# Kernel tuning notes

Measured on AMD Instinct MI355X. Metric: run time of the kernel, lower is better.

Reference implementation:

```python
import jax, jax.numpy as jnp
import numpy as np

QLEN, MLEN, BSZ, DM, NH, DH, DI = 512, 512, 8, 1024, 16, 64, 4096
KLEN = QLEN + MLEN
EPS = 1e-5
NEG = -1e30


def layer_norm(x, g, b):
    mu = jnp.mean(x, axis=-1, keepdims=True)
    var = jnp.mean(jnp.square(x - mu), axis=-1, keepdims=True)
    return (x - mu) * jax.lax.rsqrt(var + EPS) * g + b


def rel_shift(x):
    # x: [qlen, rlen, bsz, n_head] -> Transformer-XL relative shift
    q, r, b, n = x.shape
    zp = jnp.zeros((q, 1, b, n), x.dtype)
    xp = jnp.concatenate([zp, x], axis=1).reshape(r + 1, q, b, n)
    return xp[1:].reshape(q, r, b, n)


def setup_inputs() -> dict:
    key = jax.random.key(0)
    ks = jax.random.split(key, 12)
    inp = {
        "w": jax.random.normal(ks[0], (QLEN, BSZ, DM), jnp.float32),
        "r": jax.random.normal(ks[1], (KLEN, DM), jnp.float32),
        "mems": jax.random.normal(ks[2], (MLEN, BSZ, DM), jnp.float32),
        "w_qkv": jax.random.normal(ks[3], (DM, 3 * NH * DH), jnp.float32) * 0.02,
        "w_r": jax.random.normal(ks[4], (DM, NH * DH), jnp.float32) * 0.02,
        "w_o": jax.random.normal(ks[5], (NH * DH, DM), jnp.float32) * 0.02,
        "r_w_bias": jax.random.normal(ks[6], (NH, DH), jnp.float32) * 0.02,
        "r_r_bias": jax.random.normal(ks[7], (NH, DH), jnp.float32) * 0.02,
        "ln1_g": jnp.ones((DM,), jnp.float32),
        "ln1_b": jnp.zeros((DM,), jnp.float32),
        "ff_w1": jax.random.normal(ks[8], (DM, DI), jnp.float32) * 0.02,
        "ff_b1": jnp.zeros((DI,), jnp.float32),
        "ff_w2": jax.random.normal(ks[9], (DI, DM), jnp.float32) * 0.02,
        "ff_b2": jnp.zeros((DM,), jnp.float32),
        "ln2_g": jnp.ones((DM,), jnp.float32),
        "ln2_b": jnp.zeros((DM,), jnp.float32),
    }
    # causal mask with memory: query i (global pos MLEN+i) cannot attend to j > MLEN+i
    i = jnp.arange(QLEN)[:, None]
    j = jnp.arange(KLEN)[None, :]
    inp["attn_mask"] = j > (i + MLEN)
    return inp


def reference(w, r, mems, attn_mask, w_qkv, w_r, w_o, r_w_bias, r_r_bias,
              ln1_g, ln1_b, ff_w1, ff_b1, ff_w2, ff_b2, ln2_g, ln2_b):
    qlen, bsz = w.shape[0], w.shape[1]
    scale = 1.0 / (DH ** 0.5)
    cat = jnp.concatenate([mems, w], axis=0)                 # [klen, b, d]
    klen = cat.shape[0]
    heads = cat @ w_qkv                                      # [klen, b, 3*H*D]
    hq, hk, hv = jnp.split(heads, 3, axis=-1)
    hq = hq[-qlen:].reshape(qlen, bsz, NH, DH)
    hk = hk.reshape(klen, bsz, NH, DH)
    hv = hv.reshape(klen, bsz, NH, DH)
    r_head_k = (r @ w_r).reshape(klen, NH, DH)               # [rlen, H, D]

    AC = jnp.einsum('ibnd,jbnd->ijbn', hq + r_w_bias, hk)
    BD = rel_shift(jnp.einsum('ibnd,jnd->ijbn', hq + r_r_bias, r_head_k))
    score = (AC + BD) * scale                                # [q, k, b, h]
    score = jnp.where(attn_mask[:, :, None, None], NEG, score)
    prob = jax.nn.softmax(score, axis=1)
    vec = jnp.einsum('ijbn,jbnd->ibnd', prob, hv).reshape(qlen, bsz, NH * DH)
    attn_out = vec @ w_o
    h = layer_norm(w + attn_out, ln1_g, ln1_b)               # post-LN
    ff = jax.nn.relu(h @ ff_w1 + ff_b1) @ ff_w2 + ff_b2
    return layer_norm(h + ff, ln2_g, ln2_b)
```

## Files before the change

kernel.cpp:

```cpp
#include <hip/hip_runtime.h>
#include <hip/hip_bf16.h>

#define QLEN 512
#define MLEN 512
#define KLEN 1024
#define BSZ 8
#define DM 1024
#define NH 16
#define DH 64
#define DI 4096
#define NEGF (-1e30f)
#define HM_PART ((size_t)8388608)

typedef unsigned short u16;
typedef __attribute__((ext_vector_type(8))) short short8;
typedef __attribute__((ext_vector_type(4))) short s16x4;
typedef __attribute__((ext_vector_type(4))) float f32x4;

__device__ __forceinline__ float bf2f(u16 u) {
    union { unsigned i; float f; } x; x.i = ((unsigned)u) << 16; return x.f;
}
__device__ __forceinline__ u16 f2bf(float f) {
    __hip_bfloat16 h = __float2bfloat16(f);
    return *reinterpret_cast<u16*>(&h);
}
__device__ __forceinline__ float4 ldg4(const float* p) {
    return *reinterpret_cast<const float4*>(p);
}
__device__ __forceinline__ void gload16(const void* g, void* l) {
    __builtin_amdgcn_global_load_lds(
        (const __attribute__((address_space(1))) void*)g,
        (__attribute__((address_space(3))) void*)l, 16, 0, 0);
}

__global__ __launch_bounds__(256) void cast2_kernel(
    const float* __restrict__ a, const float* __restrict__ b, int splitE,
    u16* __restrict__ out, int n)
{
    int idx = (blockIdx.x * 256 + threadIdx.x) * 4;
    if (idx >= n) return;
    const float* src = (idx < splitE) ? (a + idx) : (b + (idx - splitE));
    float4 v = ldg4(src);
    u16 o[4] = { f2bf(v.x), f2bf(v.y), f2bf(v.z), f2bf(v.w) };
    *reinterpret_cast<uint2*>(&out[idx]) = *reinterpret_cast<uint2*>(o);
}

__device__ __forceinline__ void tr32(
    const float* __restrict__ W, u16* __restrict__ WT, int K, int N, int k0, int n0)
{
    __shared__ float tile[32][33];
    const int tx = threadIdx.x & 31, ty = threadIdx.x >> 5;
    #pragma unroll
    for (int j = 0; j < 4; ++j)
        tile[ty + j * 8][tx] = W[(size_t)(k0 + ty + j * 8) * N + n0 + tx];
    __syncthreads();
    #pragma unroll
    for (int j = 0; j < 4; ++j)
        WT[(size_t)(n0 + ty + j * 8) * K + k0 + tx] = f2bf(tile[tx][ty + j * 8]);
}

__global__ __launch_bounds__(256) void transpose_all(
    const float* __restrict__ w_qkv, u16* __restrict__ qkvT,
    const float* __restrict__ w_r,   u16* __restrict__ wrT,
    const float* __restrict__ w_o,   u16* __restrict__ woT,
    const float* __restrict__ ffw1,  u16* __restrict__ f1T,
    const float* __restrict__ ffw2,  u16* __restrict__ f2T)
{
    int id = blockIdx.x;
    if (id < 3072)       { int l = id;        tr32(w_qkv, qkvT, 1024, 3072, (l / 96) * 32, (l % 96) * 32); }
    else if (id < 4096)  { int l = id - 3072; tr32(w_r,   wrT,  1024, 1024, (l / 32) * 32, (l % 32) * 32); }
    else if (id < 5120)  { int l = id - 4096; tr32(w_o,   woT,  1024, 1024, (l / 32) * 32, (l % 32) * 32); }
    else if (id < 9216)  { int l = id - 5120; tr32(ffw1,  f1T,  1024, 4096, (l / 128) * 32, (l % 128) * 32); }
    else                 { int l = id - 9216; tr32(ffw2,  f2T,  4096, 1024, (l / 32) * 32, (l % 32) * 32); }
}

__global__ __launch_bounds__(256) void v_transpose(
    const u16* __restrict__ Vhm, u16* __restrict__ Vg)
{
    const int bn = blockIdx.x;
    const int kt = blockIdx.y;
    const int t = threadIdx.x;
    __shared__ u16 L[64 * 64];

    #pragma unroll
    for (int rep = 0; rep < 2; ++rep) {
        int idx = t + rep * 256;
        int key = idx >> 3, dc = (idx & 7) * 8;
        short8 v = *reinterpret_cast<const short8*>(
            &Vhm[((size_t)bn * 1024 + kt * 64 + key) * 64 + dc]);
        *reinterpret_cast<short8*>((char*)L + key * 128 + ((dc * 2) ^ ((key & 7) << 4))) = v;
    }
    __syncthreads();
    #pragma unroll
    for (int rep = 0; rep < 2; ++rep) {
        int idx = t + rep * 256;
        int d = idx >> 3, kc = (idx & 7) * 8;
        short8 o;
        #pragma unroll
        for (int e = 0; e < 8; ++e)
            o[e] = *(const short*)((char*)L + (kc + e) * 128 + ((d * 2) ^ (((kc + e) & 7) << 4)));
        *reinterpret_cast<short8*>(&Vg[((size_t)(bn * 64 + d)) * KLEN + kt * 64 + kc]) = o;
    }
}

template<bool BIAS, bool RELU, int OUT>
__global__ __launch_bounds__(256) void gemm_mfma(
    const u16* __restrict__ A, const u16* __restrict__ BT,
    const float* __restrict__ bias,
    float* __restrict__ Cf, u16* __restrict__ Cb,
    int M, int N, int K, int lda, int ldb)
{
    __shared__ u16 As[128 * 64];
    __shared__ u16 Bs[128 * 64];
    const int bm = blockIdx.y * 128, bn = blockIdx.x * 128;
    const int z = blockIdx.z;
    A  += (size_t)z * K;
    BT += (size_t)z * K;
    const size_t zoff = (size_t)z * M * N;
    const int t = threadIdx.x;
    const int w = t >> 6, l = t & 63, lg = l >> 4, lq = l & 15;
    const int wm = (w >> 1) * 64, wn = (w & 1) * 64;
    const int r8 = l >> 3, slot = l & 7;
    const int gcol = (slot * 16) ^ (r8 << 4);

    f32x4 acc[4][4];
    #pragma unroll
    for (int x = 0; x < 4; ++x)
        #pragma unroll
        for (int y = 0; y < 4; ++y)
            acc[x][y] = (f32x4){0.f, 0.f, 0.f, 0.f};

    const int swzr = (lq & 7) << 4;

    for (int k0 = 0; k0 < K; k0 += 64) {
        __syncthreads();
        #pragma unroll
        for (int it = 0; it < 4; ++it) {
            const int base_row = w * 8 + it * 32;
            gload16((const char*)A + (((size_t)(bm + base_row + r8) * lda + k0) << 1) + gcol,
                    (char*)As + base_row * 128);
            gload16((const char*)BT + (((size_t)(bn + base_row + r8) * ldb + k0) << 1) + gcol,
                    (char*)Bs + base_row * 128);
        }
        __syncthreads();
        #pragma unroll
        for (int ks = 0; ks < 2; ++ks) {
            const int cb = (ks * 64 + 16 * lg) ^ swzr;
            short8 af[4], bf_[4];
            #pragma unroll
            for (int x = 0; x < 4; ++x)
                af[x] = *reinterpret_cast<const short8*>((char*)As + (wm + 16 * x + lq) * 128 + cb);
            #pragma unroll
            for (int y = 0; y < 4; ++y)
                bf_[y] = *reinterpret_cast<const short8*>((char*)Bs + (wn + 16 * y + lq) * 128 + cb);
            #pragma unroll
            for (int x = 0; x < 4; ++x)
                #pragma unroll
                for (int y = 0; y < 4; ++y)
                    acc[x][y] = __builtin_amdgcn_mfma_f32_16x16x32_bf16(af[x], bf_[y], acc[x][y], 0, 0, 0);
        }
    }
    const int nn = ((bn + wn) >> 6) & 15;
    #pragma unroll
    for (int x = 0; x < 4; ++x) {
        #pragma unroll
        for (int y = 0; y < 4; ++y) {
            const int col = bn + wn + 16 * y + lq;
            #pragma unroll
            for (int r = 0; r < 4; ++r) {
                const int row = bm + wm + 16 * x + 4 * lg + r;
                float v = acc[x][y][r];
                if constexpr (BIAS) { if (z == 0) v += bias[col]; }
                if constexpr (RELU) v = fmaxf(v, 0.f);
                if constexpr (OUT == 0) Cf[zoff + (size_t)row * N + col] = v;
                else if constexpr (OUT == 1) Cb[zoff + (size_t)row * N + col] = f2bf(v);
                else
                    Cb[((size_t)nn * 1024 + row) * 64 + 16 * y + lq] = f2bf(v);
            }
        }
    }
}

template<bool BIAS, bool RELU, int OUT>
__global__ __launch_bounds__(512, 2) void gemm_deep(
    const u16* __restrict__ A, const u16* __restrict__ BT,
    const float* __restrict__ bias,
    float* __restrict__ Cf, u16* __restrict__ Cb,
    int M, int N, int K, int lda, int ldb)
{
    __shared__ u16 lds[3 * 24576];
    const int bm = blockIdx.y * 256, bn = blockIdx.x * 128;
    const int z = blockIdx.z;
    A  += (size_t)z * K;
    BT += (size_t)z * K;
    const size_t zoff = (size_t)z * M * N;
    const int t = threadIdx.x;
    const int w = t >> 6, l = t & 63, lg = l >> 4, lq = l & 15;
    const int wm = (w >> 1) * 64;
    const int wn = (w & 1) * 64;
    const int srow = t >> 3, slot = t & 7;
    const int gcol = (slot * 16) ^ ((srow & 7) << 4);
    const int swzr = (lq & 7) << 4;

    auto stage_tile = [&](int kt, int buf) {
        const int k0 = kt * 64;
        char* Ab = (char*)lds + buf * 49152 + w * 1024;
        char* Bb = (char*)lds + buf * 49152 + 32768 + w * 1024;
        #pragma unroll
        for (int i = 0; i < 4; ++i)
            gload16((const char*)A + (((size_t)(bm + i * 64 + srow) * lda + k0) << 1) + gcol,
                    Ab + i * 8192);
        #pragma unroll
        for (int i = 0; i < 2; ++i)
            gload16((const char*)BT + (((size_t)(bn + i * 64 + srow) * ldb + k0) << 1) + gcol,
                    Bb + i * 8192);
    };

    f32x4 acc[4][4];
    #pragma unroll
    for (int x = 0; x < 4; ++x)
        #pragma unroll
        for (int y = 0; y < 4; ++y)
            acc[x][y] = (f32x4){0.f, 0.f, 0.f, 0.f};

    const int NT = K >> 6;
    stage_tile(0, 0);
    stage_tile(1, 1);

    for (int kt = 0; kt < NT; ++kt) {
        if (kt < NT - 1) asm volatile("s_waitcnt vmcnt(6)" ::: "memory");
        else             asm volatile("s_waitcnt vmcnt(0)" ::: "memory");
        __builtin_amdgcn_s_barrier();
        __builtin_amdgcn_sched_barrier(0);
        if (kt + 2 < NT) stage_tile(kt + 2, (kt + 2) % 3);

        const char* Ab = (const char*)lds + (kt % 3) * 49152;
        const char* Bb = Ab + 32768;
        #pragma unroll
        for (int ks = 0; ks < 2; ++ks) {
            const int cb = (ks * 64 + 16 * lg) ^ swzr;
            short8 af[4], bf_[4];
            #pragma unroll
            for (int x = 0; x < 4; ++x)
                af[x] = *reinterpret_cast<const short8*>(Ab + (wm + 16 * x + lq) * 128 + cb);
            #pragma unroll
            for (int y = 0; y < 4; ++y)
                bf_[y] = *reinterpret_cast<const short8*>(Bb + (wn + 16 * y + lq) * 128 + cb);
            __builtin_amdgcn_s_setprio(1);
            #pragma unroll
            for (int x = 0; x < 4; ++x)
                #pragma unroll
                for (int y = 0; y < 4; ++y)
                    acc[x][y] = __builtin_amdgcn_mfma_f32_16x16x32_bf16(af[x], bf_[y], acc[x][y], 0, 0, 0);
            __builtin_amdgcn_s_setprio(0);
        }
    }

    const int part = (bn + wn) >> 10;
    const int nn = ((bn + wn) >> 6) & 15;
    #pragma unroll
    for (int x = 0; x < 4; ++x) {
        #pragma unroll
        for (int y = 0; y < 4; ++y) {
            const int col = bn + wn + 16 * y + lq;
            #pragma unroll
            for (int r = 0; r < 4; ++r) {
                const int row = bm + wm + 16 * x + 4 * lg + r;
                float v = acc[x][y][r];
                if constexpr (BIAS) { if (z == 0) v += bias[col]; }
                if constexpr (RELU) v = fmaxf(v, 0.f);
                if constexpr (OUT == 0) Cf[zoff + (size_t)row * N + col] = v;
                else if constexpr (OUT == 1) Cb[zoff + (size_t)row * N + col] = f2bf(v);
                else {
                    Cb[(size_t)part * HM_PART
                       + ((size_t)((row & 7) * 16 + nn) * 1024 + (row >> 3)) * 64
                       + 16 * y + lq] = f2bf(v);
                }
            }
        }
    }
}

__global__ __launch_bounds__(512, 4) void attn_mfma(
    const u16* __restrict__ Hm,
    const u16* __restrict__ Vg,
    const u16* __restrict__ rhm,
    const float* __restrict__ rwb, const float* __restrict__ rrb,
    u16* __restrict__ vec)
{
    const int bnidx = blockIdx.x;
    const int b = bnidx >> 4;
    const int n = bnidx & 15;
    const int i0 = (3 - blockIdx.y) * 128;
    const int t = threadIdx.x;
    const int w = t >> 6;
    const int l = t & 63;
    const int lg = l >> 4, lq = l & 15;
    const int r8 = l >> 3, sl = l & 7;

    const u16* Qh = Hm;
    const u16* Kh = Hm + HM_PART;

    __shared__ u16 Ks[64 * 64];
    __shared__ u16 Vt[64 * 64];
    __shared__ u16 Rs[192 * 64];
    __shared__ u16 SbO[8 * 16 * 84];
    __shared__ u16 Ps[8 * 16 * 64];

    u16* SbW = SbO + w * 16 * 84;
    u16* PsW = Ps + w * 16 * 64;
    const int swzr = (lq & 7) << 4;
    const int stg_swz = (sl * 16) ^ (r8 << 4);

    short8 qw[2], qr[2];
    {
        const size_t qbase = ((size_t)bnidx * 1024 + MLEN + i0 + 16 * w + lq) * 64;
        #pragma unroll
        for (int ks = 0; ks < 2; ++ks) {
            short8 qv = *reinterpret_cast<const short8*>(&Qh[qbase + ks * 32 + 8 * lg]);
            short8 xw, xr;
            #pragma unroll
            for (int e = 0; e < 8; ++e) {
                float f = bf2f((u16)qv[e]);
                int d = ks * 32 + 8 * lg + e;
                xw[e] = (short)f2bf(f + rwb[n * 64 + d]);
                xr[e] = (short)f2bf(f + rrb[n * 64 + d]);
            }
            qw[ks] = xw; qr[ks] = xr;
        }
    }

    float m_run = NEGF, l_run = 0.f;
    f32x4 acc[4];
    #pragma unroll
    for (int df = 0; df < 4; ++df) acc[df] = (f32x4){0.f, 0.f, 0.f, 0.f};

    const int s0 = 112 - 16 * w;
    const int rbase = 384 - i0;
    const int ntiles = i0 / 64 + 10;

    for (int tile = 0; tile < ntiles; ++tile) {
        const int j0 = tile << 6;
        __syncthreads();
        gload16((const char*)Kh + (((size_t)bnidx * 1024 + j0 + w * 8 + r8) * 64 << 1) + stg_swz,
                (char*)Ks + w * 1024);
        gload16((const char*)Vg + ((((size_t)bnidx * 64 + w * 8 + r8) * KLEN + j0) << 1) + stg_swz,
                (char*)Vt + w * 1024);
        if (tile == 0) {
            #pragma unroll
            for (int pass = 0; pass < 3; ++pass) {
                int row = pass * 64 + w * 8 + r8;
                int o = rbase + row;
                o = o > (KLEN - 1) ? (KLEN - 1) : o;
                gload16((const char*)rhm + (((size_t)n * 1024 + o) * 64 << 1) + stg_swz,
                        (char*)Rs + pass * 8192 + w * 1024);
            }
        } else {
            const int g = tile + 2;
            int o = rbase + g * 64 + w * 8 + r8;
            o = o > (KLEN - 1) ? (KLEN - 1) : o;
            gload16((const char*)rhm + (((size_t)n * 1024 + o) * 64 << 1) + stg_swz,
                    (char*)Rs + (g % 3) * 8192 + w * 1024);
        }
        __syncthreads();

        const int bmax = i0 + 16 * w + 15 + MLEN - j0;
        if (bmax < 0) continue;

        __builtin_amdgcn_s_setprio(1);
        #pragma unroll
        for (int ff = 0; ff < 5; ++ff) {
            const int olf = s0 + 16 * ff;
            const int srowb = ((tile + (olf >> 6)) % 3) * 64 + (olf & 63);
            f32x4 d = (f32x4){0.f, 0.f, 0.f, 0.f};
            #pragma unroll
            for (int ks = 0; ks < 2; ++ks) {
                short8 a = *reinterpret_cast<const short8*>(
                    (char*)Rs + (srowb + lq) * 128 + ((ks * 64 + 16 * lg) ^ swzr));
                d = __builtin_amdgcn_mfma_f32_16x16x32_bf16(a, qr[ks], d, 0, 0, 0);
            }
            s16x4 pk;
            #pragma unroll
            for (int r = 0; r < 4; ++r) pk[r] = (short)f2bf(d[r]);
            *reinterpret_cast<s16x4*>(&SbW[lq * 84 + 16 * ff + 4 * lg]) = pk;
        }
        f32x4 dac[4];
        #pragma unroll
        for (int f = 0; f < 4; ++f) {
            f32x4 d = (f32x4){0.f, 0.f, 0.f, 0.f};
            #pragma unroll
            for (int ks = 0; ks < 2; ++ks) {
                short8 a = *reinterpret_cast<const short8*>(
                    (char*)Ks + (16 * f + lq) * 128 + ((ks * 64 + 16 * lg) ^ swzr));
                d = __builtin_amdgcn_mfma_f32_16x16x32_bf16(a, qw[ks], d, 0, 0, 0);
            }
            dac[f] = d;
        }
        __builtin_amdgcn_s_setprio(0);

        const bool fullTile = (i0 + 16 * w + MLEN - j0) >= 63;
        float sv[4][4];
        float mx = NEGF;
        if (fullTile) {
            #pragma unroll
            for (int f = 0; f < 4; ++f)
                #pragma unroll
                for (int r = 0; r < 4; ++r) {
                    int k = 16 * f + 4 * lg + r;
                    float bd = bf2f(SbW[lq * 84 + k - lq + 15]);
                    float x = (dac[f][r] + bd) * 0.125f;
                    sv[f][r] = x;
                    mx = fmaxf(mx, x);
                }
        } else {
            const int bound = i0 + 16 * w + lq + MLEN - j0;
            #pragma unroll
            for (int f = 0; f < 4; ++f)
                #pragma unroll
                for (int r = 0; r < 4; ++r) {
                    int k = 16 * f + 4 * lg + r;
                    float bd = bf2f(SbW[lq * 84 + k - lq + 15]);
                    float x = (k <= bound) ? (dac[f][r] + bd) * 0.125f : NEGF;
                    sv[f][r] = x;
                    mx = fmaxf(mx, x);
                }
        }
        mx = fmaxf(mx, __shfl_xor(mx, 16));
        mx = fmaxf(mx, __shfl_xor(mx, 32));
        const bool defer = (__all(mx <= m_run + 8.0f) != 0);
        const float m_new = defer ? m_run : fmaxf(m_run, mx);
        float ps = 0.f;
        #pragma unroll
        for (int f = 0; f < 4; ++f) {
            s16x4 pk;
            #pragma unroll
            for (int r = 0; r < 4; ++r) {
                float p = __expf(sv[f][r] - m_new);
                ps += p;
                pk[r] = (short)f2bf(p);
            }
            *reinterpret_cast<s16x4*>(
                (char*)PsW + lq * 128 + (((4 * f + lg) ^ ((lq & 7) << 1)) << 3)) = pk;
        }
        ps += __shfl_xor(ps, 16);
        ps += __shfl_xor(ps, 32);
        if (defer) {
            l_run += ps;
        } else {
            float alpha = __expf(m_run - m_new);
            l_run = l_run * alpha + ps;
            m_run = m_new;
            float alr[4];
            #pragma unroll
            for (int r = 0; r < 4; ++r) alr[r] = __shfl(alpha, 20 * lg + r);
            #pragma unroll
            for (int df = 0; df < 4; ++df)
                #pragma unroll
                for (int r = 0; r < 4; ++r) acc[df][r] *= alr[r];
        }

        __builtin_amdgcn_s_setprio(1);
        #pragma unroll
        for (int df = 0; df < 4; ++df) {
            f32x4 a = acc[df];
            #pragma unroll
            for (int ks = 0; ks < 2; ++ks) {
                short8 pa = *reinterpret_cast<const short8*>(
                    (char*)PsW + lq * 128 + ((ks * 64 + 16 * lg) ^ swzr));
                short8 vb = *reinterpret_cast<const short8*>(
                    (char*)Vt + (16 * df + lq) * 128 + ((ks * 64 + 16 * lg) ^ swzr));
                a = __builtin_amdgcn_mfma_f32_16x16x32_bf16(pa, vb, a, 0, 0, 0);
            }
            acc[df] = a;
        }
        __builtin_amdgcn_s_setprio(0);
    }

    float inv[4];
    #pragma unroll
    for (int r = 0; r < 4; ++r) inv[r] = 1.f / __shfl(l_run, 20 * lg + r);
    #pragma unroll
    for (int df = 0; df < 4; ++df) {
        #pragma unroll
        for (int r = 0; r < 4; ++r) {
            const int il = 16 * w + 4 * lg + r;
            float o = acc[df][r] * inv[r];
            vec[((size_t)((i0 + il) * BSZ + b)) * DM + n * 64 + 16 * df + lq] = f2bf(o);
        }
    }
}

template<int NRES, bool WB>
__global__ __launch_bounds__(256) void ln_res_kernel(
    const float* __restrict__ x, const float* __restrict__ res,
    const float* __restrict__ res2,
    const float* __restrict__ g, const float* __restrict__ bta,
    float* __restrict__ out, u16* __restrict__ outb)
{
    const int row = blockIdx.x;
    const int t = threadIdx.x;
    const int lane = t & 63, wv = t >> 6;
    __shared__ float red0[4], red1[4];

    float4 a = ldg4(&x[(size_t)row * DM + t * 4]);
    float4 b = ldg4(&res[(size_t)row * DM + t * 4]);
    float v0 = a.x + b.x, v1 = a.y + b.y, v2 = a.z + b.z, v3 = a.w + b.w;
    if constexpr (NRES == 2) {
        float4 c = ldg4(&res2[(size_t)row * DM + t * 4]);
        v0 += c.x; v1 += c.y; v2 += c.z; v3 += c.w;
    }
    float s = v0 + v1 + v2 + v3;
    #pragma unroll
    for (int o = 32; o; o >>= 1) s += __shfl_xor(s, o);
    if (lane == 0) red0[wv] = s;
    __syncthreads();
    float mu = (red0[0] + red0[1] + red0[2] + red0[3]) * (1.f / DM);
    float d0 = v0 - mu, d1 = v1 - mu, d2 = v2 - mu, d3 = v3 - mu;
    float q = d0*d0 + d1*d1 + d2*d2 + d3*d3;
    #pragma unroll
    for (int o = 32; o; o >>= 1) q += __shfl_xor(q, o);
    if (lane == 0) red1[wv] = q;
    __syncthreads();
    float var = (red1[0] + red1[1] + red1[2] + red1[3]) * (1.f / DM);
    float rs = rsqrtf(var + 1e-5f);
    float4 gv = ldg4(&g[t * 4]);
    float4 bv = ldg4(&bta[t * 4]);
    float o0 = d0 * rs * gv.x + bv.x;
    float o1 = d1 * rs * gv.y + bv.y;
    float o2 = d2 * rs * gv.z + bv.z;
    float o3 = d3 * rs * gv.w + bv.w;
    float4 o4 = make_float4(o0, o1, o2, o3);
    *reinterpret_cast<float4*>(&out[(size_t)row * DM + t * 4]) = o4;
    if constexpr (WB) {
        u16 ob[4] = { f2bf(o0), f2bf(o1), f2bf(o2), f2bf(o3) };
        *reinterpret_cast<uint2*>(&outb[(size_t)row * DM + t * 4]) = *reinterpret_cast<uint2*>(ob);
    }
}

extern "C" void kernel_launch(void* const* d_in, const int* in_sizes, int n_in,
                              void* d_out, int out_size, void* d_ws, size_t ws_size,
                              hipStream_t stream) {
    const float* w     = (const float*)d_in[0];
    const float* r     = (const float*)d_in[1];
    const float* mems  = (const float*)d_in[2];
    const float* w_qkv = (const float*)d_in[3];
    const float* w_r   = (const float*)d_in[4];
    const float* w_o   = (const float*)d_in[5];
    const float* rwb   = (const float*)d_in[6];
    const float* rrb   = (const float*)d_in[7];
    const float* ln1g  = (const float*)d_in[8];
    const float* ln1b  = (const float*)d_in[9];
    const float* ffw1  = (const float*)d_in[10];
    const float* ffb1  = (const float*)d_in[11];
    const float* ffw2  = (const float*)d_in[12];
    const float* ffb2  = (const float*)d_in[13];
    const float* ln2g  = (const float*)d_in[14];
    const float* ln2b  = (const float*)d_in[15];
    (void)in_sizes; (void)n_in; (void)out_size; (void)ws_size;

    char* p = (char*)d_ws;
    auto alloc = [&](size_t bytes) { char* q = p; p += (bytes + 255) & ~(size_t)255; return q; };
    u16* catB   = (u16*)alloc((size_t)8192 * 1024 * 2);
    u16* rB     = (u16*)alloc((size_t)1024 * 1024 * 2);
    u16* qkvT   = (u16*)alloc((size_t)3072 * 1024 * 2);
    u16* wrT    = (u16*)alloc((size_t)1024 * 1024 * 2);
    u16* woT    = (u16*)alloc((size_t)1024 * 1024 * 2);
    u16* f1T    = (u16*)alloc((size_t)4096 * 1024 * 2);
    u16* f2T    = (u16*)alloc((size_t)1024 * 4096 * 2);
    u16* headsHm= (u16*)alloc((size_t)3 * HM_PART * 2);
    u16* rhkHm  = (u16*)alloc((size_t)1024 * 1024 * 2);
    u16* vec    = (u16*)alloc((size_t)4096 * 1024 * 2);
    u16* hB     = (u16*)alloc((size_t)4096 * 1024 * 2);
    u16* ff1    = (u16*)alloc((size_t)4096 * 4096 * 2);
    float* hF   = (float*)alloc((size_t)4096 * 1024 * 4);

    u16* Vg = catB;
    float* attn_out = (float*)ff1;
    float* ff2 = (float*)headsHm;
    float* outp = (float*)d_out;

    cast2_kernel<<<8192, 256, 0, stream>>>(mems, w, 4096 * 1024, catB, 8192 * 1024);
    cast2_kernel<<<1024, 256, 0, stream>>>(r, r, 1024 * 1024, rB, 1024 * 1024);
    transpose_all<<<13312, 256, 0, stream>>>(w_qkv, qkvT, w_r, wrT, w_o, woT,
                                             ffw1, f1T, ffw2, f2T);

    gemm_deep<false, false, 2><<<dim3(24, 32), 512, 0, stream>>>(
        catB, qkvT, nullptr, nullptr, headsHm, 8192, 3072, 1024, 1024, 1024);
    v_transpose<<<dim3(128, 16), 256, 0, stream>>>(headsHm + 2 * HM_PART, Vg);
    gemm_mfma<false, false, 3><<<dim3(8, 8), 256, 0, stream>>>(
        rB, wrT, nullptr, nullptr, rhkHm, 1024, 1024, 1024, 1024, 1024);
    attn_mfma<<<dim3(BSZ * NH, QLEN / 128), 512, 0, stream>>>(
        headsHm, Vg, rhkHm, rwb, rrb, vec);
    gemm_mfma<false, false, 0><<<dim3(8, 32, 2), 256, 0, stream>>>(
        vec, woT, nullptr, attn_out, nullptr, 4096, 1024, 512, 1024, 1024);
    ln_res_kernel<2, true><<<4096, 256, 0, stream>>>(
        w, attn_out, attn_out + (size_t)4096 * 1024, ln1g, ln1b, hF, hB);
    gemm_deep<true, true, 1><<<dim3(32, 16), 512, 0, stream>>>(
        hB, f1T, ffb1, nullptr, ff1, 4096, 4096, 1024, 1024, 1024);
    gemm_deep<true, false, 0><<<dim3(8, 16, 2), 512, 0, stream>>>(
        ff1, f2T, ffb2, ff2, nullptr, 4096, 1024, 2048, 4096, 4096);
    ln_res_kernel<2, false><<<4096, 256, 0, stream>>>(
        hF, ff2, ff2 + (size_t)4096 * 1024, ln2g, ln2b, outp, nullptr);
}
```

Before: 327.0 us.

## Add 256x256 tiled GEMM, skip unused QKV tiles, merge cast kernels

Adds a new gemm256 kernel with 256x256 output tiles, double-buffered LDS, and global loads interleaved with the MFMA phases. It is used for the QKV projection and the FF1 GEMM. For QKV it launches only the tiles that are needed: Q for the last 512 rows and K/V for all rows. The original gemm_deep computed Q for the memory rows too, and those results were never used. The two cast launches are merged into one. The larger tiles raise register and LDS pressure (launch bounds 512,2), and a 256-block FF1 grid gives only about one wave of blocks on the device.

Result: faster. 313.4 us (-4.2%).

```diff
diff --git a/kernel.cpp b/kernel.cpp
--- a/kernel.cpp
+++ b/kernel.cpp
@@ -33,16 +33,25 @@
         (__attribute__((address_space(3))) void*)l, 16, 0, 0);
 }
 
-__global__ __launch_bounds__(256) void cast2_kernel(
-    const float* __restrict__ a, const float* __restrict__ b, int splitE,
-    u16* __restrict__ out, int n)
+__global__ __launch_bounds__(256) void cast_all(
+    const float* __restrict__ mems, const float* __restrict__ w,
+    const float* __restrict__ r, u16* __restrict__ catB, u16* __restrict__ rB)
 {
     int idx = (blockIdx.x * 256 + threadIdx.x) * 4;
-    if (idx >= n) return;
-    const float* src = (idx < splitE) ? (a + idx) : (b + (idx - splitE));
+    const float* src;
+    u16* dst;
+    if (idx < 8388608) {
+        src = (idx < 4194304) ? (mems + idx) : (w + idx - 4194304);
+        dst = catB + idx;
+    } else {
+        int i2 = idx - 8388608;
+        if (i2 >= 1048576) return;
+        src = r + i2;
+        dst = rB + i2;
+    }
     float4 v = ldg4(src);
     u16 o[4] = { f2bf(v.x), f2bf(v.y), f2bf(v.z), f2bf(v.w) };
-    *reinterpret_cast<uint2*>(&out[idx]) = *reinterpret_cast<uint2*>(o);
+    *reinterpret_cast<uint2*>(dst) = *reinterpret_cast<uint2*>(o);
 }
 
 __device__ __forceinline__ void tr32(
@@ -256,8 +265,6 @@
         }
     }
 
-    const int part = (bn + wn) >> 10;
-    const int nn = ((bn + wn) >> 6) & 15;
     #pragma unroll
     for (int x = 0; x < 4; ++x) {
         #pragma unroll
@@ -270,11 +277,126 @@
                 if constexpr (BIAS) { if (z == 0) v += bias[col]; }
                 if constexpr (RELU) v = fmaxf(v, 0.f);
                 if constexpr (OUT == 0) Cf[zoff + (size_t)row * N + col] = v;
-                else if constexpr (OUT == 1) Cb[zoff + (size_t)row * N + col] = f2bf(v);
-                else {
+                else Cb[zoff + (size_t)row * N + col] = f2bf(v);
+            }
+        }
+    }
+}
+
+template<bool BIAS, bool RELU, int OUT>
+__global__ __launch_bounds__(512, 2) void gemm256(
+    const u16* __restrict__ A, const u16* __restrict__ BT,
+    const float* __restrict__ bias, u16* __restrict__ Cb,
+    int N, int K, int lda, int ldb, int nbx)
+{
+    __shared__ u16 lds[2 * 32768];
+    int bm, bn;
+    if constexpr (OUT == 2) {
+        const int id = blockIdx.x;
+        if (id < 64) { bm = 4096 + (id >> 2) * 256; bn = (id & 3) * 256; }
+        else         { int j = id - 64; bm = (j >> 3) * 256; bn = 1024 + (j & 7) * 256; }
+    } else {
+        bm = (blockIdx.x / nbx) * 256; bn = (blockIdx.x % nbx) * 256;
+    }
+    const int t = threadIdx.x;
+    const int w = t >> 6, l = t & 63, lg = l >> 4, lq = l & 15;
+    const int wm = (w >> 2) * 128;
+    const int wn = (w & 3) * 64;
+    const int srow = t >> 3, slot = t & 7;
+    const int gcol = (slot * 16) ^ ((srow & 7) << 4);
+    const int swzr = (lq & 7) << 4;
+
+    auto stage_pair = [&](int kt, char* buf, int ph) {
+        const int k0 = kt * 64;
+        if (ph < 2) {
+            #pragma unroll
+            for (int i = 0; i < 2; ++i) {
+                int g = ph * 2 + i;
+                gload16((const char*)A + (((size_t)(bm + g * 64 + srow) * lda + k0) << 1) + gcol,
+                        buf + g * 8192 + w * 1024);
+            }
+        } else {
+            #pragma unroll
+            for (int i = 0; i < 2; ++i) {
+                int g = (ph - 2) * 2 + i;
+                gload16((const char*)BT + (((size_t)(bn + g * 64 + srow) * ldb + k0) << 1) + gcol,
+                        buf + 32768 + g * 8192 + w * 1024);
+            }
+        }
+    };
+
+    f32x4 acc[8][4];
+    #pragma unroll
+    for (int m = 0; m < 8; ++m)
+        #pragma unroll
+        for (int y = 0; y < 4; ++y)
+            acc[m][y] = (f32x4){0.f, 0.f, 0.f, 0.f};
+
+    const int NT = K >> 6;
+    #pragma unroll
+    for (int ph = 0; ph < 4; ++ph) stage_pair(0, (char*)lds, ph);
+
+    for (int kt = 0; kt < NT; ++kt) {
+        asm volatile("s_waitcnt vmcnt(0)" ::: "memory");
+        __builtin_amdgcn_s_barrier();
+        __builtin_amdgcn_sched_barrier(0);
+
+        const char* Ab = (const char*)lds + (kt & 1) * 65536;
+        const char* Bb = Ab + 32768;
+        char* nbuf = (char*)lds + ((kt + 1) & 1) * 65536;
+        const bool pf = (kt + 1 < NT);
+
+        short8 bf_[4];
+        #pragma unroll
+        for (int ks = 0; ks < 2; ++ks) {
+            const int cb = (ks * 64 + 16 * lg) ^ swzr;
+            #pragma unroll
+            for (int mh = 0; mh < 2; ++mh) {
+                short8 af[4];
+                if (mh == 0) {
+                    #pragma unroll
+                    for (int y = 0; y < 4; ++y)
+                        bf_[y] = *reinterpret_cast<const short8*>(Bb + (wn + 16 * y + lq) * 128 + cb);
+                }
+                #pragma unroll
+                for (int x = 0; x < 4; ++x)
+                    af[x] = *reinterpret_cast<const short8*>(
+                        Ab + (wm + mh * 64 + 16 * x + lq) * 128 + cb);
+                if (pf) stage_pair(kt + 1, nbuf, ks * 2 + mh);
+                __builtin_amdgcn_s_barrier();
+                asm volatile("s_waitcnt lgkmcnt(0)" ::: "memory");
+                __builtin_amdgcn_sched_barrier(0);
+                __builtin_amdgcn_s_setprio(1);
+                #pragma unroll
+                for (int x = 0; x < 4; ++x)
+                    #pragma unroll
+                    for (int y = 0; y < 4; ++y)
+                        acc[mh * 4 + x][y] = __builtin_amdgcn_mfma_f32_16x16x32_bf16(
+                            af[x], bf_[y], acc[mh * 4 + x][y], 0, 0, 0);
+                __builtin_amdgcn_s_setprio(0);
+                __builtin_amdgcn_s_barrier();
+            }
+        }
+    }
+
+    #pragma unroll
+    for (int m = 0; m < 8; ++m) {
+        #pragma unroll
+        for (int y = 0; y < 4; ++y) {
+            const int col = bn + wn + 16 * y + lq;
+            #pragma unroll
+            for (int r = 0; r < 4; ++r) {
+                const int row = bm + wm + m * 16 + 4 * lg + r;
+                float v = acc[m][y][r];
+                if constexpr (BIAS) v += bias[col];
+                if constexpr (RELU) v = fmaxf(v, 0.f);
+                if constexpr (OUT == 2) {
+                    const int part = col >> 10, nn = (col >> 6) & 15;
                     Cb[(size_t)part * HM_PART
                        + ((size_t)((row & 7) * 16 + nn) * 1024 + (row >> 3)) * 64
-                       + 16 * y + lq] = f2bf(v);
+                       + (col & 63)] = f2bf(v);
+                } else {
+                    Cb[(size_t)row * N + col] = f2bf(v);
                 }
             }
         }
@@ -579,13 +701,12 @@
     float* ff2 = (float*)headsHm;
     float* outp = (float*)d_out;
 
-    cast2_kernel<<<8192, 256, 0, stream>>>(mems, w, 4096 * 1024, catB, 8192 * 1024);
-    cast2_kernel<<<1024, 256, 0, stream>>>(r, r, 1024 * 1024, rB, 1024 * 1024);
+    cast_all<<<9216, 256, 0, stream>>>(mems, w, r, catB, rB);
     transpose_all<<<13312, 256, 0, stream>>>(w_qkv, qkvT, w_r, wrT, w_o, woT,
                                              ffw1, f1T, ffw2, f2T);
 
-    gemm_deep<false, false, 2><<<dim3(24, 32), 512, 0, stream>>>(
-        catB, qkvT, nullptr, nullptr, headsHm, 8192, 3072, 1024, 1024, 1024);
+    gemm256<false, false, 2><<<320, 512, 0, stream>>>(
+        catB, qkvT, nullptr, headsHm, 3072, 1024, 1024, 1024, 0);
     v_transpose<<<dim3(128, 16), 256, 0, stream>>>(headsHm + 2 * HM_PART, Vg);
     gemm_mfma<false, false, 3><<<dim3(8, 8), 256, 0, stream>>>(
         rB, wrT, nullptr, nullptr, rhkHm, 1024, 1024, 1024, 1024, 1024);
@@ -595,8 +716,8 @@
         vec, woT, nullptr, attn_out, nullptr, 4096, 1024, 512, 1024, 1024);
     ln_res_kernel<2, true><<<4096, 256, 0, stream>>>(
         w, attn_out, attn_out + (size_t)4096 * 1024, ln1g, ln1b, hF, hB);
-    gemm_deep<true, true, 1><<<dim3(32, 16), 512, 0, stream>>>(
-        hB, f1T, ffb1, nullptr, ff1, 4096, 4096, 1024, 1024, 1024);
+    gemm256<true, true, 1><<<256, 512, 0, stream>>>(
+        hB, f1T, ffb1, ff1, 4096, 1024, 1024, 1024, 16);
     gemm_deep<true, false, 0><<<dim3(8, 16, 2), 512, 0, stream>>>(
         ff1, f2T, ffb2, ff2, nullptr, 4096, 1024, 2048, 4096, 4096);
     ln_res_kernel<2, false><<<4096, 256, 0, stream>>>(
```
